# Optimization experiments

Measured on AMD Instinct MI355X. Metric: run time of the kernel, lower is better.

## Reference

```python
import jax, jax.numpy as jnp
import numpy as np

B, S, D, H = 8, 1024, 1024, 16
HD = D // H  # head_size = 64


def layernorm(x, g, b, eps=1e-5):
    mu = jnp.mean(x, axis=-1, keepdims=True)
    var = jnp.var(x, axis=-1, keepdims=True)
    return (x - mu) * jax.lax.rsqrt(var + eps) * g + b


def setup_inputs() -> dict:
    key = jax.random.key(0)
    ks = jax.random.split(key, 12)
    s_attn = 1.0 / np.sqrt(D)
    inp = {
        "x": jax.random.normal(ks[0], (B, S, D), dtype=jnp.float32),
        # per-head q/k/v projections (bias=False), stacked: [H, D, HD]
        "Wq": jax.random.normal(ks[1], (H, D, HD), dtype=jnp.float32) * s_attn,
        "Wk": jax.random.normal(ks[2], (H, D, HD), dtype=jnp.float32) * s_attn,
        "Wv": jax.random.normal(ks[3], (H, D, HD), dtype=jnp.float32) * s_attn,
        "Wo": jax.random.normal(ks[4], (D, D), dtype=jnp.float32) * s_attn,
        "bo": jnp.zeros((D,), dtype=jnp.float32),
        # FFN: hidden = 1 * n_embd (as in source)
        "W1": jax.random.normal(ks[5], (D, D), dtype=jnp.float32) * s_attn,
        "b1": jnp.zeros((D,), dtype=jnp.float32),
        "W2": jax.random.normal(ks[6], (D, D), dtype=jnp.float32) * s_attn,
        "b2": jnp.zeros((D,), dtype=jnp.float32),
        "g_ln1": jnp.ones((D,), dtype=jnp.float32),
        "b_ln1": jnp.zeros((D,), dtype=jnp.float32),
        "g_ln2": jnp.ones((D,), dtype=jnp.float32),
        "b_ln2": jnp.zeros((D,), dtype=jnp.float32),
    }
    return inp


def reference(x, Wq, Wk, Wv, Wo, bo, W1, b1, W2, b2, g_ln1, b_ln1, g_ln2, b_ln2):
    # pre-LN self-attention
    h = layernorm(x, g_ln1, b_ln1)
    q = jnp.einsum("bsd,hde->bhse", h, Wq)
    k = jnp.einsum("bsd,hde->bhse", h, Wk)
    v = jnp.einsum("bsd,hde->bhse", h, Wv)
    scale = HD ** -0.5  # k.shape[-1] ** -0.5
    wei = jax.nn.softmax(jnp.einsum("bhse,bhte->bhst", q, k) * scale, axis=-1)
    attn = jnp.einsum("bhst,bhte->bhse", wei, v)  # [B,H,S,HD]
    # concat heads (head order matches torch.cat over head list)
    attn = attn.transpose(0, 2, 1, 3).reshape(B, S, D)
    sa = attn @ Wo + bo
    x = x + sa
    # pre-LN FFN with exact GELU (torch nn.GELU default)
    h2 = layernorm(x, g_ln2, b_ln2)
    ff = jax.nn.gelu(h2 @ W1 + b1, approximate=False) @ W2 + b2
    return x + ff
```

## Files before the change

### kernel.cpp

```cpp
#include <hip/hip_runtime.h>
#include <hip/hip_bf16.h>
#include <math.h>

#define B_ 8
#define S_ 1024
#define D_ 1024
#define H_ 16
#define HD_ 64

typedef __bf16 bf16x8 __attribute__((ext_vector_type(8)));
typedef __bf16 bf16x4 __attribute__((ext_vector_type(4)));
typedef float f32x4 __attribute__((ext_vector_type(4)));

#define FMAX3(a, b, c) fmaxf(fmaxf((a), (b)), (c))

__device__ __forceinline__ void gld_lds16(const __bf16* g, __bf16* l) {
  __builtin_amdgcn_global_load_lds(
      (const __attribute__((address_space(1))) void*)g,
      (__attribute__((address_space(3))) void*)l, 16, 0, 0);
}

__global__ __launch_bounds__(256) void ln_f32(const float* __restrict__ x,
                                              const float* __restrict__ g,
                                              const float* __restrict__ b,
                                              __bf16* __restrict__ out) {
  int row = blockIdx.x;
  const float* xr = x + (size_t)row * D_;
  __bf16* outr = out + (size_t)row * D_;
  int tid = threadIdx.x;

  float4 v = ((const float4*)xr)[tid];
  float s = v.x + v.y + v.z + v.w;
  float ss = v.x * v.x + v.y * v.y + v.z * v.z + v.w * v.w;

  #pragma unroll
  for (int m = 1; m < 64; m <<= 1) {
    s += __shfl_xor(s, m);
    ss += __shfl_xor(ss, m);
  }
  __shared__ float red[10];
  int wid = tid >> 6;
  if ((tid & 63) == 0) { red[wid] = s; red[4 + wid] = ss; }
  __syncthreads();
  if (tid == 0) {
    float ts = red[0] + red[1] + red[2] + red[3];
    float tss = red[4] + red[5] + red[6] + red[7];
    float mu = ts * (1.0f / D_);
    float var = tss * (1.0f / D_) - mu * mu;
    red[8] = mu;
    red[9] = rsqrtf(var + 1e-5f);
  }
  __syncthreads();
  float mu = red[8], rstd = red[9];
  float4 gv = ((const float4*)g)[tid];
  float4 bv = ((const float4*)b)[tid];
  bf16x4 o;
  o[0] = (__bf16)((v.x - mu) * rstd * gv.x + bv.x);
  o[1] = (__bf16)((v.y - mu) * rstd * gv.y + bv.y);
  o[2] = (__bf16)((v.z - mu) * rstd * gv.z + bv.z);
  o[3] = (__bf16)((v.w - mu) * rstd * gv.w + bv.w);
  *(bf16x4*)(outr + tid * 4) = o;
}

__global__ __launch_bounds__(256) void ln_bf16(const __bf16* __restrict__ x,
                                               const float* __restrict__ g,
                                               const float* __restrict__ b,
                                               __bf16* __restrict__ out) {
  int row = blockIdx.x;
  const __bf16* xr = x + (size_t)row * D_;
  __bf16* outr = out + (size_t)row * D_;
  int tid = threadIdx.x;

  bf16x4 xv = *(const bf16x4*)(xr + tid * 4);
  float v0 = (float)xv[0], v1 = (float)xv[1], v2 = (float)xv[2], v3 = (float)xv[3];
  float s = v0 + v1 + v2 + v3;
  float ss = v0 * v0 + v1 * v1 + v2 * v2 + v3 * v3;

  #pragma unroll
  for (int m = 1; m < 64; m <<= 1) {
    s += __shfl_xor(s, m);
    ss += __shfl_xor(ss, m);
  }
  __shared__ float red[10];
  int wid = tid >> 6;
  if ((tid & 63) == 0) { red[wid] = s; red[4 + wid] = ss; }
  __syncthreads();
  if (tid == 0) {
    float ts = red[0] + red[1] + red[2] + red[3];
    float tss = red[4] + red[5] + red[6] + red[7];
    float mu = ts * (1.0f / D_);
    float var = tss * (1.0f / D_) - mu * mu;
    red[8] = mu;
    red[9] = rsqrtf(var + 1e-5f);
  }
  __syncthreads();
  float mu = red[8], rstd = red[9];
  float4 gv = ((const float4*)g)[tid];
  float4 bv = ((const float4*)b)[tid];
  bf16x4 o;
  o[0] = (__bf16)((v0 - mu) * rstd * gv.x + bv.x);
  o[1] = (__bf16)((v1 - mu) * rstd * gv.y + bv.y);
  o[2] = (__bf16)((v2 - mu) * rstd * gv.z + bv.z);
  o[3] = (__bf16)((v3 - mu) * rstd * gv.w + bv.w);
  *(bf16x4*)(outr + tid * 4) = o;
}

__global__ __launch_bounds__(256) void transpose_all(const float* __restrict__ Wq,
                                                     const float* __restrict__ Wk,
                                                     const float* __restrict__ Wv,
                                                     const float* __restrict__ Wo,
                                                     const float* __restrict__ W1,
                                                     const float* __restrict__ W2,
                                                     __bf16* __restrict__ out) {
  __shared__ float t[64][65];
  const int x = blockIdx.x, y = blockIdx.y, z = blockIdx.z;
  const int tid = threadIdx.x;
  const int r = tid >> 4, c4 = (tid & 15) * 4;

  const float* src;
  int stride, orowbase, kbase;
  if (z < 3) {
    const float* W = (z == 0 ? Wq : z == 1 ? Wk : Wv);
    src = W + (size_t)y * (D_ * HD_) + (size_t)(x * 64) * HD_;
    stride = HD_;
    orowbase = z * 1024 + y * 64;
    kbase = x * 64;
  } else {
    const float* W = (z == 3 ? Wo : z == 4 ? W1 : W2);
    src = W + (size_t)(y * 64) * D_ + x * 64;
    stride = D_;
    orowbase = z * 1024 + x * 64;
    kbase = y * 64;
  }

  #pragma unroll
  for (int i = 0; i < 4; ++i) {
    float4 v = *(const float4*)&src[(size_t)(i * 16 + r) * stride + c4];
    t[i * 16 + r][c4 + 0] = v.x;
    t[i * 16 + r][c4 + 1] = v.y;
    t[i * 16 + r][c4 + 2] = v.z;
    t[i * 16 + r][c4 + 3] = v.w;
  }
  __syncthreads();
  #pragma unroll
  for (int i = 0; i < 4; ++i) {
    bf16x4 o;
    #pragma unroll
    for (int j = 0; j < 4; ++j) o[j] = (__bf16)t[c4 + j][i * 16 + r];
    *(bf16x4*)&out[(size_t)(orowbase + i * 16 + r) * 1024 + kbase + c4] = o;
  }
}

#define MODE_QKV 0
#define MODE_PROJ 1
#define MODE_FF1 2
#define MODE_FF2 3

#define QSCALE 0.18033688011112042f

template <int MODE>
__global__ __launch_bounds__(256) void gemm_mfma(const __bf16* __restrict__ A,
                                                 const __bf16* __restrict__ Bt,
                                                 const float* __restrict__ bias,
                                                 const float* __restrict__ residf,
                                                 const __bf16* __restrict__ residb,
                                                 float* __restrict__ outf,
                                                 __bf16* __restrict__ outb,
                                                 int M, int N, int K) {
  __shared__ __align__(16) __bf16 As[128 * 64];
  __shared__ __align__(16) __bf16 Bs[128 * 64];
  const int tid = threadIdx.x;

  const int gx = (int)gridDim.x;
  const int nwg = gx * (int)gridDim.y;
  const int flat = (int)blockIdx.y * gx + (int)blockIdx.x;
  const int wg = (flat & 7) * (nwg >> 3) + (flat >> 3);
  const int m0 = (wg / gx) * 128, n0 = (wg % gx) * 128;

  const int w = tid >> 6, l = tid & 63, lr = l & 15, lg = l >> 4;
  const int wm = (w >> 1) * 64, wn = (w & 1) * 64;

  f32x4 acc[4][4] = {};

  for (int k0 = 0; k0 < K; k0 += 64) {
    __syncthreads();
    #pragma unroll
    for (int i = 0; i < 4; ++i) {
      int e = i * 256 + tid;
      int row = e >> 3;
      int col = ((e & 7) ^ (row & 7)) * 8;
      gld_lds16(A + (size_t)(m0 + row) * K + k0 + col, &As[e * 8]);
    }
    #pragma unroll
    for (int i = 0; i < 4; ++i) {
      int e = i * 256 + tid;
      int row = e >> 3;
      int col = ((e & 7) ^ (row & 7)) * 8;
      gld_lds16(Bt + (size_t)(n0 + row) * K + k0 + col, &Bs[e * 8]);
    }
    asm volatile("s_waitcnt vmcnt(0)");
    __syncthreads();

    #pragma unroll
    for (int kk = 0; kk < 2; ++kk) {
      bf16x8 af[4], bfr[4];
      #pragma unroll
      for (int i = 0; i < 4; ++i)
        af[i] = *(const bf16x8*)
            &As[((wm + i * 16 + lr) * 8 + ((kk * 4 + lg) ^ (lr & 7))) * 8];
      #pragma unroll
      for (int j = 0; j < 4; ++j)
        bfr[j] = *(const bf16x8*)
            &Bs[((wn + j * 16 + lr) * 8 + ((kk * 4 + lg) ^ (lr & 7))) * 8];
      #pragma unroll
      for (int i = 0; i < 4; ++i)
        #pragma unroll
        for (int j = 0; j < 4; ++j)
          acc[i][j] = __builtin_amdgcn_mfma_f32_16x16x32_bf16(af[i], bfr[j], acc[i][j], 0, 0, 0);
    }
  }

  #pragma unroll
  for (int i = 0; i < 4; ++i) {
    #pragma unroll
    for (int j = 0; j < 4; ++j) {
      #pragma unroll
      for (int r = 0; r < 4; ++r) {
        int m = m0 + wm + i * 16 + 4 * lg + r;
        int n = n0 + wn + j * 16 + lr;
        float val = acc[i][j][r];
        if (MODE == MODE_QKV) {
          int b = m >> 10, s = m & 1023;
          int which = n >> 10, hh = (n >> 6) & 15, e = n & 63;
          if (which == 0) val *= QSCALE;
          outb[(size_t)which * 8388608 + ((size_t)(b * 16 + hh) * 1024 + s) * 64 + e] =
              (__bf16)val;
        } else if (MODE == MODE_PROJ) {
          size_t idx = (size_t)m * 1024 + n;
          outb[idx] = (__bf16)(residf[idx] + val + bias[n]);
        } else if (MODE == MODE_FF1) {
          val += bias[n];
          outb[(size_t)m * 1024 + n] =
              (__bf16)(0.5f * val * (1.0f + erff(val * 0.70710678118654752f)));
        } else {
          size_t idx = (size_t)m * 1024 + n;
          outf[idx] = (float)residb[idx] + val + bias[n];
        }
      }
    }
  }
}

__global__ __launch_bounds__(512) void fattn(const __bf16* __restrict__ q,
                                             const __bf16* __restrict__ k,
                                             const __bf16* __restrict__ v,
                                             __bf16* __restrict__ outC) {
  __shared__ __align__(16) __bf16 Klds[2][64 * 64];
  __shared__ __align__(16) __bf16 Vp[2][64 * 64];

  const int bid = blockIdx.x;
  const int bh = (bid & 7) * 16 + ((bid >> 3) & 15);
  const int qt = bid >> 7;
  const int tid = threadIdx.x;
  const int w = tid >> 6, l = tid & 63;
  const int lr = l & 15, lg = l >> 4;

  const size_t base = (size_t)bh * (S_ * HD_);
  const int qrow0 = qt * 128 + w * 16;
  const __bf16* kg = k + base;
  const __bf16* vg = v + base;

  const int krow = tid >> 3;
  const int kcol = ((tid & 7) ^ (krow & 7)) * 8;
  const int vc = (l & 0x20) + ((l & 0xC) << 1) + ((l & 0x10) >> 2) + (l & 3);
  const int vchi = vc >> 3, vclo = vc & 7;

  bf16x8 qf0, qf1;
  {
    const __bf16* qp = q + base + (size_t)(qrow0 + lr) * HD_ + lg * 8;
    qf0 = *(const bf16x8*)(qp);
    qf1 = *(const bf16x8*)(qp + 32);
  }

  const __bf16 onev = (lr == 0) ? (__bf16)1.0f : (__bf16)0.0f;
  const bf16x8 vones = {onev, onev, onev, onev, onev, onev, onev, onev};

  f32x4 oacc[5] = {};
  float m_run = -1e30f;

  gld_lds16(kg + (size_t)krow * HD_ + kcol, &Klds[0][tid * 8]);
  bf16x8 vr;
  {
    vr = *(const bf16x8*)(vg + (size_t)l * HD_ + w * 8);
    #pragma unroll
    for (int i = 0; i < 8; ++i)
      Vp[0][(w * 8 + i) * 64 + ((vchi ^ i) << 3) + vclo] = vr[i];
    vr = *(const bf16x8*)(vg + (size_t)(64 + l) * HD_ + w * 8);
  }
  asm volatile("s_waitcnt vmcnt(1) lgkmcnt(0)" ::: "memory");
  __builtin_amdgcn_sched_barrier(0);
  __builtin_amdgcn_s_barrier();
  __builtin_amdgcn_sched_barrier(0);

  int cur = 0;
  for (int t = 0; t < 16; ++t) {
    {
      int tn = (t < 15) ? (t + 1) : 15;
      gld_lds16(kg + ((size_t)tn * 64 + krow) * HD_ + kcol, &Klds[cur ^ 1][tid * 8]);
    }

    f32x4 sacc[4];
    const __bf16* kb = &Klds[cur][0];
    __builtin_amdgcn_s_setprio(1);
    #pragma unroll
    for (int g = 0; g < 4; ++g) {
      bf16x8 kf0 = *(const bf16x8*)&kb[((16 * g + lr) * 8 + (lg ^ (lr & 7))) * 8];
      bf16x8 kf1 = *(const bf16x8*)&kb[((16 * g + lr) * 8 + ((lg + 4) ^ (lr & 7))) * 8];
      f32x4 z = {0.f, 0.f, 0.f, 0.f};
      z = __builtin_amdgcn_mfma_f32_16x16x32_bf16(kf0, qf0, z, 0, 0, 0);
      sacc[g] = __builtin_amdgcn_mfma_f32_16x16x32_bf16(kf1, qf1, z, 0, 0, 0);
    }
    __builtin_amdgcn_s_setprio(0);

    #pragma unroll
    for (int i = 0; i < 8; ++i)
      Vp[cur ^ 1][(w * 8 + i) * 64 + ((vchi ^ i) << 3) + vclo] = vr[i];
    {
      int tnn = (t < 14) ? (t + 2) : 15;
      vr = *(const bf16x8*)(vg + ((size_t)tnn * 64 + l) * HD_ + w * 8);
    }

    float m0 = FMAX3(sacc[0][0], sacc[0][1], sacc[0][2]);
    float m1 = FMAX3(sacc[0][3], sacc[1][0], sacc[1][1]);
    float m2 = FMAX3(sacc[1][2], sacc[1][3], sacc[2][0]);
    float m3 = FMAX3(sacc[2][1], sacc[2][2], sacc[2][3]);
    float m4 = FMAX3(sacc[3][0], sacc[3][1], sacc[3][2]);
    float tm = FMAX3(FMAX3(m0, m1, m2), FMAX3(m3, m4, sacc[3][3]), m_run);
    tm = fmaxf(tm, __shfl_xor(tm, 16));
    tm = fmaxf(tm, __shfl_xor(tm, 32));

    if (!__all(tm - m_run <= 11.5f)) {
      float corr = __builtin_amdgcn_exp2f(m_run - tm);
      m_run = tm;
      #pragma unroll
      for (int r = 0; r < 4; ++r) {
        float cq = __shfl(corr, 4 * lg + r);
        #pragma unroll
        for (int g = 0; g < 5; ++g) oacc[g][r] *= cq;
      }
    }

    float p[4][4];
    #pragma unroll
    for (int g = 0; g < 4; ++g)
      #pragma unroll
      for (int r = 0; r < 4; ++r)
        p[g][r] = __builtin_amdgcn_exp2f(sacc[g][r] - m_run);

    bf16x8 af0, af1;
    #pragma unroll
    for (int j = 0; j < 8; ++j) {
      af0[j] = (__bf16)p[j >> 2][j & 3];
      af1[j] = (__bf16)p[2 + (j >> 2)][j & 3];
    }
    __builtin_amdgcn_s_setprio(1);
    #pragma unroll
    for (int g = 0; g < 4; ++g) {
      bf16x8 vf0 = *(const bf16x8*)&Vp[cur][(16 * g + lr) * 64 + ((lg ^ (lr & 7)) << 3)];
      bf16x8 vf1 = *(const bf16x8*)&Vp[cur][(16 * g + lr) * 64 + (((lg + 4) ^ (lr & 7)) << 3)];
      oacc[g] = __builtin_amdgcn_mfma_f32_16x16x32_bf16(af0, vf0, oacc[g], 0, 0, 0);
      oacc[g] = __builtin_amdgcn_mfma_f32_16x16x32_bf16(af1, vf1, oacc[g], 0, 0, 0);
    }
    oacc[4] = __builtin_amdgcn_mfma_f32_16x16x32_bf16(af0, vones, oacc[4], 0, 0, 0);
    oacc[4] = __builtin_amdgcn_mfma_f32_16x16x32_bf16(af1, vones, oacc[4], 0, 0, 0);
    __builtin_amdgcn_s_setprio(0);

    asm volatile("s_waitcnt vmcnt(1) lgkmcnt(0)" ::: "memory");
    __builtin_amdgcn_sched_barrier(0);
    __builtin_amdgcn_s_barrier();
    __builtin_amdgcn_sched_barrier(0);
    cur ^= 1;
  }

  const int b = bh >> 4, hh = bh & 15;
  #pragma unroll
  for (int r = 0; r < 4; ++r) {
    float linv = 1.0f / __shfl(oacc[4][r], l & 48);
    int srow = qrow0 + 4 * lg + r;
    __bf16* op = outC + ((size_t)(b * S_ + srow)) * D_ + hh * HD_;
    #pragma unroll
    for (int g = 0; g < 4; ++g) op[16 * g + lr] = (__bf16)(oacc[g][r] * linv);
  }
}

extern "C" void kernel_launch(void* const* d_in, const int* in_sizes, int n_in,
                              void* d_out, int out_size, void* d_ws, size_t ws_size,
                              hipStream_t stream) {
  const float* x   = (const float*)d_in[0];
  const float* Wq  = (const float*)d_in[1];
  const float* Wk  = (const float*)d_in[2];
  const float* Wv  = (const float*)d_in[3];
  const float* Wo  = (const float*)d_in[4];
  const float* bo  = (const float*)d_in[5];
  const float* W1  = (const float*)d_in[6];
  const float* b1  = (const float*)d_in[7];
  const float* W2  = (const float*)d_in[8];
  const float* b2  = (const float*)d_in[9];
  const float* g1  = (const float*)d_in[10];
  const float* bl1 = (const float*)d_in[11];
  const float* g2  = (const float*)d_in[12];
  const float* bl2 = (const float*)d_in[13];
  float* out = (float*)d_out;

  const size_t MN = (size_t)B_ * S_ * D_;
  __bf16* h     = (__bf16*)d_ws;
  __bf16* wt    = h + MN;
  __bf16* qkv   = wt + (size_t)6144 * 1024;
  __bf16* attnC = qkv + 3 * MN;
  __bf16* ff1   = attnC + MN;
  __bf16* mid   = ff1 + MN;

  __bf16* wqkv_t = wt;
  __bf16* wo_t   = wt + (size_t)3072 * 1024;
  __bf16* w1_t   = wt + (size_t)4096 * 1024;
  __bf16* w2_t   = wt + (size_t)5120 * 1024;

  const int rows = B_ * S_;

  ln_f32<<<rows, 256, 0, stream>>>(x, g1, bl1, h);
  transpose_all<<<dim3(16, 16, 6), 256, 0, stream>>>(Wq, Wk, Wv, Wo, W1, W2, wt);

  gemm_mfma<MODE_QKV><<<dim3(24, 64), 256, 0, stream>>>(
      h, wqkv_t, nullptr, nullptr, nullptr, nullptr, qkv, rows, 3072, D_);
  fattn<<<1024, 512, 0, stream>>>(qkv, qkv + MN, qkv + 2 * MN, attnC);
  gemm_mfma<MODE_PROJ><<<dim3(8, 64), 256, 0, stream>>>(
      attnC, wo_t, bo, x, nullptr, nullptr, mid, rows, D_, D_);
  ln_bf16<<<rows, 256, 0, stream>>>(mid, g2, bl2, h);
  gemm_mfma<MODE_FF1><<<dim3(8, 64), 256, 0, stream>>>(
      h, w1_t, b1, nullptr, nullptr, nullptr, ff1, rows, D_, D_);
  gemm_mfma<MODE_FF2><<<dim3(8, 64), 256, 0, stream>>>(
      ff1, w2_t, b2, nullptr, mid, out, nullptr, rows, D_, D_);
}
```

Baseline: 234.4 us.

## Double-buffer LDS tiles in MFMA GEMM to overlap loads with compute

```diff
diff --git a/kernel.cpp b/kernel.cpp
--- a/kernel.cpp
+++ b/kernel.cpp
@@ -167,8 +167,8 @@
                                                  float* __restrict__ outf,
                                                  __bf16* __restrict__ outb,
                                                  int M, int N, int K) {
-  __shared__ __align__(16) __bf16 As[128 * 64];
-  __shared__ __align__(16) __bf16 Bs[128 * 64];
+  __shared__ __align__(16) __bf16 As[2][128 * 64];
+  __shared__ __align__(16) __bf16 Bs[2][128 * 64];
   const int tid = threadIdx.x;
 
   const int gx = (int)gridDim.x;
@@ -182,42 +182,65 @@
 
   f32x4 acc[4][4] = {};
 
-  for (int k0 = 0; k0 < K; k0 += 64) {
-    __syncthreads();
+  auto stage = [&](int buf, int k0) {
     #pragma unroll
     for (int i = 0; i < 4; ++i) {
       int e = i * 256 + tid;
       int row = e >> 3;
       int col = ((e & 7) ^ (row & 7)) * 8;
-      gld_lds16(A + (size_t)(m0 + row) * K + k0 + col, &As[e * 8]);
+      gld_lds16(A + (size_t)(m0 + row) * K + k0 + col, &As[buf][e * 8]);
     }
     #pragma unroll
     for (int i = 0; i < 4; ++i) {
       int e = i * 256 + tid;
       int row = e >> 3;
       int col = ((e & 7) ^ (row & 7)) * 8;
-      gld_lds16(Bt + (size_t)(n0 + row) * K + k0 + col, &Bs[e * 8]);
-    }
-    asm volatile("s_waitcnt vmcnt(0)");
-    __syncthreads();
-
+      gld_lds16(Bt + (size_t)(n0 + row) * K + k0 + col, &Bs[buf][e * 8]);
+    }
+  };
+
+  auto compute = [&](int buf) {
     #pragma unroll
     for (int kk = 0; kk < 2; ++kk) {
       bf16x8 af[4], bfr[4];
       #pragma unroll
       for (int i = 0; i < 4; ++i)
         af[i] = *(const bf16x8*)
-            &As[((wm + i * 16 + lr) * 8 + ((kk * 4 + lg) ^ (lr & 7))) * 8];
+            &As[buf][((wm + i * 16 + lr) * 8 + ((kk * 4 + lg) ^ (lr & 7))) * 8];
       #pragma unroll
       for (int j = 0; j < 4; ++j)
         bfr[j] = *(const bf16x8*)
-            &Bs[((wn + j * 16 + lr) * 8 + ((kk * 4 + lg) ^ (lr & 7))) * 8];
+            &Bs[buf][((wn + j * 16 + lr) * 8 + ((kk * 4 + lg) ^ (lr & 7))) * 8];
       #pragma unroll
       for (int i = 0; i < 4; ++i)
         #pragma unroll
         for (int j = 0; j < 4; ++j)
           acc[i][j] = __builtin_amdgcn_mfma_f32_16x16x32_bf16(af[i], bfr[j], acc[i][j], 0, 0, 0);
     }
+  };
+
+  const int NT = K >> 6;
+  stage(0, 0);
+  asm volatile("s_waitcnt vmcnt(0)" ::: "memory");
+  __builtin_amdgcn_sched_barrier(0);
+  __builtin_amdgcn_s_barrier();
+  __builtin_amdgcn_sched_barrier(0);
+
+  for (int t = 0; t < NT; t += 2) {
+    stage(1, (t + 1) * 64);
+    compute(0);
+    asm volatile("s_waitcnt vmcnt(0)" ::: "memory");
+    __builtin_amdgcn_sched_barrier(0);
+    __builtin_amdgcn_s_barrier();
+    __builtin_amdgcn_sched_barrier(0);
+
+    int tn = (t + 2 < NT) ? (t + 2) : (NT - 1);
+    stage(0, tn * 64);
+    compute(1);
+    asm volatile("s_waitcnt vmcnt(0)" ::: "memory");
+    __builtin_amdgcn_sched_barrier(0);
+    __builtin_amdgcn_s_barrier();
+    __builtin_amdgcn_sched_barrier(0);
   }
 
   #pragma unroll
```

Result: no change. 238.3 us (+1.7%).
